# Optimization experiments

Hardware: AMD Instinct MI355X
Metric: run time of the kernel (lower is better)

Reference implementation:

```python
import jax, jax.numpy as jnp
import numpy as np

K = 5  # kensize -> kernel is (2K+1) x (2K+1) = 11x11


def _box_kernels(k):
    r = k
    s = 2 * r + 1
    M13 = np.concatenate([np.ones([r + 1, s]), np.zeros([r, s])], axis=0)  # top half (y1)
    M23 = np.concatenate([np.zeros([r, s]), np.ones([r + 1, s])], axis=0)  # bottom half (y2)
    M11 = np.concatenate([np.ones([s, r + 1]), np.zeros([s, r])], axis=1)  # left half (x1)
    M21 = np.concatenate([np.zeros([s, r]), np.ones([s, r + 1])], axis=1)  # right half (x2)
    to = lambda m: jnp.asarray(m, dtype=jnp.float32).reshape(1, 1, s, s)  # OIHW
    return to(M11), to(M21), to(M13), to(M23)


def setup_inputs() -> dict:
    key = jax.random.key(0)
    x = jax.random.uniform(key, (64, 1, 512, 512), dtype=jnp.float32)
    wx1, wx2, wy1, wy2 = _box_kernels(K)
    return {"x": x, "wx1": wx1, "wx2": wx2, "wy1": wy1, "wy2": wy2}


def _conv(x, w):
    return jax.lax.conv_general_dilated(
        x, w, window_strides=(1, 1), padding="VALID",
        dimension_numbers=("NCHW", "OIHW", "NCHW"))


def reference(x, wx1, wx2, wy1, wy2):
    # reflect-pad by K on H and W, then shift by 0.01 so box sums are > 0
    xp = jnp.pad(x, ((0, 0), (0, 0), (K, K), (K, K)), mode="reflect") + 0.01
    gx1 = _conv(xp, wx1)
    gx2 = _conv(xp, wx2)
    gy1 = _conv(xp, wy1)
    gy2 = _conv(xp, wy2)
    gx = jnp.log(gx1 / gx2)
    gy = jnp.log(gy1 / gy2)
    # L2 norm over the stacked (gx, gy) pair -> [B,1,H,W]
    return jnp.sqrt(gx * gx + gy * gy)
```

## Files before the change

### kernel.cpp

```cpp
#include <hip/hip_runtime.h>
#include <hip/hip_fp16.h>


#define N   512
#define SH  80
#define LN2 0.69314718056f

typedef __fp16 h2  __attribute__((ext_vector_type(2)));
typedef __fp16 h4v __attribute__((ext_vector_type(4)));
typedef __fp16 h8v __attribute__((ext_vector_type(8)));

__device__ __forceinline__ float2 f2add(float2 a, float2 b){ return make_float2(a.x+b.x, a.y+b.y); }
__device__ __forceinline__ float2 f2sub(float2 a, float2 b){ return make_float2(a.x-b.x, a.y-b.y); }

__device__ __forceinline__ void load20(const __half* __restrict__ arr, int base, float* __restrict__ t) {
    h8v a = *(const h8v*)(arr + base);
    h8v b = *(const h8v*)(arr + base + 8);
    h4v c = *(const h4v*)(arr + base + 16);
    #pragma unroll
    for (int j = 0; j < 8; ++j) t[j]      = (float)a[j];
    #pragma unroll
    for (int j = 0; j < 8; ++j) t[8 + j]  = (float)b[j];
    #pragma unroll
    for (int j = 0; j < 4; ++j) t[16 + j] = (float)c[j];
}

__global__ __launch_bounds__(64, 6) void boxlog_kernel(
    const float* __restrict__ x, float* __restrict__ out)
{
    __shared__ __align__(16) __half S6A [21*SH];
    __shared__ __align__(16) __half fulA[16*SH];

    const int lane = threadIdx.x;
    const int wg  = blockIdx.x;
    const int sw  = (wg & 7) * 2048 + (wg >> 3);
    const int bz  = sw >> 8;
    const int rem = sw & 255;
    const int by  = rem >> 3;
    const int bx  = rem & 7;
    const int X0 = bx * 64, Y0 = by * 16;
    const float* __restrict__ xb   = x   + (size_t)bz * ((size_t)N * N);
    float* __restrict__       outb = out + (size_t)bz * ((size_t)N * N);

    if (lane < 38) {
        const int gc = X0 - 6 + 2 * lane;

        auto body = [&](auto loadrow) {
            float2 t[26];
            #pragma unroll
            for (int j = 0; j < 11; ++j) t[j] = loadrow(j);
            float2 lo = f2add(f2add(f2add(t[0],t[1]), f2add(t[2],t[3])), f2add(t[4],t[5]));
            float2 hi = f2add(f2add(f2add(t[5],t[6]), f2add(t[7],t[8])), f2add(t[9],t[10]));
            {
                float2 fu = f2sub(f2add(lo, hi), t[5]);
                *(h2*)&S6A [2 * lane] = __builtin_amdgcn_cvt_pkrtz(lo.x + 0.06f, lo.y + 0.06f);
                *(h2*)&fulA[2 * lane] = __builtin_amdgcn_cvt_pkrtz(fu.x + 0.11f, fu.y + 0.11f);
            }
            #pragma unroll
            for (int k = 1; k < 21; ++k) {
                if (k < 16) t[k+10] = loadrow(k + 10);
                lo = f2sub(f2add(lo, t[k+5]), t[k-1]);
                *(h2*)&S6A[k * SH + 2 * lane] = __builtin_amdgcn_cvt_pkrtz(lo.x + 0.06f, lo.y + 0.06f);
                if (k < 16) {
                    hi = f2sub(f2add(hi, t[k+10]), t[k+4]);
                    float2 fu = f2sub(f2add(lo, hi), t[k+5]);
                    *(h2*)&fulA[k * SH + 2 * lane] = __builtin_amdgcn_cvt_pkrtz(fu.x + 0.11f, fu.y + 0.11f);
                }
            }
        };

        if (by >= 1 && by <= 30 && bx >= 1 && bx <= 6) {
            body([&](int j) {
                return *(const float2*)(xb + (size_t)(Y0 - 5 + j) * N + gc);
            });
        } else {
            const bool vec = (gc >= 0) && (gc <= N - 2);
            body([&](int j) {
                int gr = Y0 - 5 + j;
                gr = gr < 0 ? -gr : (gr > N-1 ? 2*(N-1) - gr : gr);
                const float* rowp = xb + (size_t)gr * N;
                if (vec) return *(const float2*)(rowp + gc);
                int c0 = gc, c1 = gc + 1;
                c0 = c0 < 0 ? -c0 : (c0 > N-1 ? 2*(N-1) - c0 : c0);
                c1 = c1 < 0 ? -c1 : (c1 > N-1 ? 2*(N-1) - c1 : c1);
                return make_float2(rowp[c0], rowp[c1]);
            });
        }
    }
    __syncthreads();

    const int tx = lane & 7;
    const int ty = lane >> 3;
    #pragma unroll
    for (int s = 0; s < 2; ++s) {
        const int row  = ty + 8 * s;
        const int base = row * SH + 8 * tx;

        float gy1[8], ly[8];
        {
            float t[20];
            load20(S6A, base, t);
            float g = ((t[1]+t[2])+(t[3]+t[4]))+((t[5]+t[6])+(t[7]+t[8]))+((t[9]+t[10])+t[11]);
            gy1[0] = g;
            #pragma unroll
            for (int p = 1; p < 8; ++p) { g += t[p+11] - t[p]; gy1[p] = g; }
        }
        {
            float t[20];
            load20(S6A, base + 5*SH, t);
            float g = ((t[1]+t[2])+(t[3]+t[4]))+((t[5]+t[6])+(t[7]+t[8]))+((t[9]+t[10])+t[11]);
            ly[0] = __builtin_amdgcn_logf(gy1[0]) - __builtin_amdgcn_logf(g);
            #pragma unroll
            for (int p = 1; p < 8; ++p) {
                g += t[p+11] - t[p];
                ly[p] = __builtin_amdgcn_logf(gy1[p]) - __builtin_amdgcn_logf(g);
            }
        }
        {
            float t[20];
            load20(fulA, base, t);
            float g1 = ((t[1]+t[2])+(t[3]+t[4]))+(t[5]+t[6]);
            float g2 = ((t[6]+t[7])+(t[8]+t[9]))+(t[10]+t[11]);
            float r8[8];
            #pragma unroll
            for (int p = 0; p < 8; ++p) {
                if (p) {
                    g1 += t[p+6]  - t[p];
                    g2 += t[p+11] - t[p+5];
                }
                float lx = __builtin_amdgcn_logf(g1) - __builtin_amdgcn_logf(g2);
                r8[p] = LN2 * __builtin_amdgcn_sqrtf(lx*lx + ly[p]*ly[p]);
            }
            float* op = outb + (size_t)(Y0 + row) * N + X0 + tx * 8;
            *(float4*)op       = make_float4(r8[0], r8[1], r8[2], r8[3]);
            *(float4*)(op + 4) = make_float4(r8[4], r8[5], r8[6], r8[7]);
        }
    }
}

extern "C" void kernel_launch(void* const* d_in, const int* in_sizes, int n_in,
                              void* d_out, int out_size, void* d_ws, size_t ws_size,
                              hipStream_t stream) {
    const float* x = (const float*)d_in[0];
    float* out = (float*)d_out;
    dim3 grid(8 * 32 * 64);
    dim3 block(64);
    boxlog_kernel<<<grid, block, 0, stream>>>(x, out);
}
```

Before: 33.30 us.

## Share per-row log values via LDS to cut redundant log evaluations

Instead of computing log of both the top and bottom vertical box sums for every output, each row's log-sum is computed once (21 rows), written as floats into an aliased LDS buffer, and reused for the partner row five rows below. Horizontal logs are computed once per 13-wide window and reused as differences lS[p]-lS[p+5]. This removes duplicate transcendental work, at the cost of an extra barrier pair, more LDS, more registers, and launch bounds lowered from 6 to 4 waves.

```diff
diff --git a/kernel.cpp b/kernel.cpp
--- a/kernel.cpp
+++ b/kernel.cpp
@@ -4,6 +4,7 @@
 
 #define N   512
 #define SH  80
+#define MS  68
 #define LN2 0.69314718056f
 
 typedef __fp16 h2  __attribute__((ext_vector_type(2)));
@@ -25,11 +26,13 @@
     for (int j = 0; j < 4; ++j) t[16 + j] = (float)c[j];
 }
 
-__global__ __launch_bounds__(64, 6) void boxlog_kernel(
+__global__ __launch_bounds__(64, 4) void boxlog_kernel(
     const float* __restrict__ x, float* __restrict__ out)
 {
-    __shared__ __align__(16) __half S6A [21*SH];
-    __shared__ __align__(16) __half fulA[16*SH];
+    __shared__ __align__(16) unsigned char reg1[21 * MS * 4];
+    __shared__ __align__(16) __half fulA[16 * SH];
+    __half* S6A = (__half*)reg1;
+    float*  Mld = (float*)reg1;
 
     const int lane = threadIdx.x;
     const int wg  = blockIdx.x;
@@ -52,9 +55,9 @@
             float2 lo = f2add(f2add(f2add(t[0],t[1]), f2add(t[2],t[3])), f2add(t[4],t[5]));
             float2 hi = f2add(f2add(f2add(t[5],t[6]), f2add(t[7],t[8])), f2add(t[9],t[10]));
             {
-                float2 fu = f2sub(f2add(lo, hi), t[5]);
+                float2 fv = f2sub(f2add(lo, hi), t[5]);
                 *(h2*)&S6A [2 * lane] = __builtin_amdgcn_cvt_pkrtz(lo.x + 0.06f, lo.y + 0.06f);
-                *(h2*)&fulA[2 * lane] = __builtin_amdgcn_cvt_pkrtz(fu.x + 0.11f, fu.y + 0.11f);
+                *(h2*)&fulA[2 * lane] = __builtin_amdgcn_cvt_pkrtz(fv.x + 0.11f, fv.y + 0.11f);
             }
             #pragma unroll
             for (int k = 1; k < 21; ++k) {
@@ -63,8 +66,8 @@
                 *(h2*)&S6A[k * SH + 2 * lane] = __builtin_amdgcn_cvt_pkrtz(lo.x + 0.06f, lo.y + 0.06f);
                 if (k < 16) {
                     hi = f2sub(f2add(hi, t[k+10]), t[k+4]);
-                    float2 fu = f2sub(f2add(lo, hi), t[k+5]);
-                    *(h2*)&fulA[k * SH + 2 * lane] = __builtin_amdgcn_cvt_pkrtz(fu.x + 0.11f, fu.y + 0.11f);
+                    float2 fv = f2sub(f2add(lo, hi), t[k+5]);
+                    *(h2*)&fulA[k * SH + 2 * lane] = __builtin_amdgcn_cvt_pkrtz(fv.x + 0.11f, fv.y + 0.11f);
                 }
             }
         };
@@ -91,51 +94,61 @@
 
     const int tx = lane & 7;
     const int ty = lane >> 3;
-    #pragma unroll
-    for (int s = 0; s < 2; ++s) {
-        const int row  = ty + 8 * s;
-        const int base = row * SH + 8 * tx;
 
-        float gy1[8], ly[8];
-        {
-            float t[20];
-            load20(S6A, base, t);
-            float g = ((t[1]+t[2])+(t[3]+t[4]))+((t[5]+t[6])+(t[7]+t[8]))+((t[9]+t[10])+t[11]);
-            gy1[0] = g;
-            #pragma unroll
-            for (int p = 1; p < 8; ++p) { g += t[p+11] - t[p]; gy1[p] = g; }
+    float Ma[8], Mb[8], Mc[8];
+    auto mchunk = [&](int r, float* __restrict__ m) {
+        float t[20];
+        load20(S6A, r * SH + 8 * tx, t);
+        float g = ((t[1]+t[2])+(t[3]+t[4]))+((t[5]+t[6])+(t[7]+t[8]))+((t[9]+t[10])+t[11]);
+        m[0] = __builtin_amdgcn_logf(g);
+        #pragma unroll
+        for (int p = 1; p < 8; ++p) { g += t[p+11] - t[p]; m[p] = __builtin_amdgcn_logf(g); }
+    };
+    mchunk(ty, Ma);
+    mchunk(ty + 8, Mb);
+    if (ty < 5) mchunk(ty + 16, Mc);
+
+    float La[13], Lb[13];
+    auto lchunk = [&](int r, float* __restrict__ l) {
+        float t[20];
+        load20(fulA, r * SH + 8 * tx, t);
+        float g = ((t[1]+t[2])+(t[3]+t[4]))+(t[5]+t[6]);
+        l[0] = __builtin_amdgcn_logf(g);
+        #pragma unroll
+        for (int p = 1; p < 13; ++p) { g += t[p+6] - t[p]; l[p] = __builtin_amdgcn_logf(g); }
+    };
+    lchunk(ty, La);
+    lchunk(ty + 8, Lb);
+
+    __syncthreads();
+
+    *(float4*)&Mld[ty * MS + 8 * tx]           = make_float4(Ma[0], Ma[1], Ma[2], Ma[3]);
+    *(float4*)&Mld[ty * MS + 8 * tx + 4]       = make_float4(Ma[4], Ma[5], Ma[6], Ma[7]);
+    *(float4*)&Mld[(ty + 8) * MS + 8 * tx]     = make_float4(Mb[0], Mb[1], Mb[2], Mb[3]);
+    *(float4*)&Mld[(ty + 8) * MS + 8 * tx + 4] = make_float4(Mb[4], Mb[5], Mb[6], Mb[7]);
+    if (ty < 5) {
+        *(float4*)&Mld[(ty + 16) * MS + 8 * tx]     = make_float4(Mc[0], Mc[1], Mc[2], Mc[3]);
+        *(float4*)&Mld[(ty + 16) * MS + 8 * tx + 4] = make_float4(Mc[4], Mc[5], Mc[6], Mc[7]);
+    }
+    __syncthreads();
+
+    auto strip = [&](int row, const float* __restrict__ mS, const float* __restrict__ lS) {
+        float mB[8];
+        *(float4*)&mB[0] = *(const float4*)&Mld[(row + 5) * MS + 8 * tx];
+        *(float4*)&mB[4] = *(const float4*)&Mld[(row + 5) * MS + 8 * tx + 4];
+        float r8[8];
+        #pragma unroll
+        for (int p = 0; p < 8; ++p) {
+            float ly = mS[p] - mB[p];
+            float lx = lS[p] - lS[p + 5];
+            r8[p] = LN2 * __builtin_amdgcn_sqrtf(lx * lx + ly * ly);
         }
-        {
-            float t[20];
-            load20(S6A, base + 5*SH, t);
-            float g = ((t[1]+t[2])+(t[3]+t[4]))+((t[5]+t[6])+(t[7]+t[8]))+((t[9]+t[10])+t[11]);
-            ly[0] = __builtin_amdgcn_logf(gy1[0]) - __builtin_amdgcn_logf(g);
-            #pragma unroll
-            for (int p = 1; p < 8; ++p) {
-                g += t[p+11] - t[p];
-                ly[p] = __builtin_amdgcn_logf(gy1[p]) - __builtin_amdgcn_logf(g);
-            }
-        }
-        {
-            float t[20];
-            load20(fulA, base, t);
-            float g1 = ((t[1]+t[2])+(t[3]+t[4]))+(t[5]+t[6]);
-            float g2 = ((t[6]+t[7])+(t[8]+t[9]))+(t[10]+t[11]);
-            float r8[8];
-            #pragma unroll
-            for (int p = 0; p < 8; ++p) {
-                if (p) {
-                    g1 += t[p+6]  - t[p];
-                    g2 += t[p+11] - t[p+5];
-                }
-                float lx = __builtin_amdgcn_logf(g1) - __builtin_amdgcn_logf(g2);
-                r8[p] = LN2 * __builtin_amdgcn_sqrtf(lx*lx + ly[p]*ly[p]);
-            }
-            float* op = outb + (size_t)(Y0 + row) * N + X0 + tx * 8;
-            *(float4*)op       = make_float4(r8[0], r8[1], r8[2], r8[3]);
-            *(float4*)(op + 4) = make_float4(r8[4], r8[5], r8[6], r8[7]);
-        }
-    }
+        float* op = outb + (size_t)(Y0 + row) * N + X0 + tx * 8;
+        *(float4*)op       = make_float4(r8[0], r8[1], r8[2], r8[3]);
+        *(float4*)(op + 4) = make_float4(r8[4], r8[5], r8[6], r8[7]);
+    };
+    strip(ty,     Ma, La);
+    strip(ty + 8, Mb, Lb);
 }
 
 extern "C" void kernel_launch(void* const* d_in, const int* in_sizes, int n_in,
```

Measured after the change: 34.60 us. 3.9% more time.
